# Kernel tuning notes

Measured on AMD Instinct MI355X. Metric: run time of the kernel, lower is better.

## Reference

```python
import jax, jax.numpy as jnp
import numpy as np

NH = 16
NKV = 4
ROPE_BASE = 10000.0
ROPE_TSL = 1024
EPS = 1.1920928955078125e-07  # torch fp32 finfo eps (F.rms_norm default)


def _rms_norm(t):
    return t * jax.lax.rsqrt(jnp.mean(t * t, axis=-1, keepdims=True) + EPS)


def _rope_tables(T, hd):
    # Rotary with rd = hd (rope_dims=0 -> full-head rope). NTK rescale if T > tsl.
    rd = hd
    if T > ROPE_TSL:
        base = ROPE_BASE * (T / ROPE_TSL) ** (rd / (rd - 2))
    else:
        base = ROPE_BASE
    inv_freq = 1.0 / base ** (np.arange(0, rd, 2, dtype=np.float32) / rd)
    t = np.arange(T, dtype=np.float32)
    fr = np.outer(t, inv_freq)  # [T, hd//2]
    return jnp.asarray(np.cos(fr)), jnp.asarray(np.sin(fr))


def _apply_rope(x, cos, sin):
    # x: [B,T,H,D]; cos/sin: [T, D//2] broadcast over batch & heads
    h = x.shape[-1] // 2
    x1, x2 = x[..., :h], x[..., h:]
    c = cos[None, :, None, :]
    s = sin[None, :, None, :]
    return jnp.concatenate((x1 * c + x2 * s, -x1 * s + x2 * c), axis=-1)


def setup_inputs() -> dict:
    key = jax.random.key(0)
    k1, k2, k3, k4, k5 = jax.random.split(key, 5)
    B, T, dim = 2, 2048, 2048
    hd = dim // NH
    kd = NKV * hd
    std = 0.02
    return {
        "x": jax.random.normal(k1, (B, T, dim), dtype=jnp.float32),
        "Wq": jax.random.normal(k2, (dim, dim), dtype=jnp.float32) * std,
        "Wk": jax.random.normal(k3, (kd, dim), dtype=jnp.float32) * std,
        "Wv": jax.random.normal(k4, (kd, dim), dtype=jnp.float32) * std,
        "Wp": jax.random.normal(k5, (dim, dim), dtype=jnp.float32) * std,
        "q_gain": jnp.full((NH,), 1.5, dtype=jnp.float32),
    }


def reference(x, Wq, Wk, Wv, Wp, q_gain):
    B, T, d = x.shape
    hd = d // NH
    g = NH // NKV
    q = (x @ Wq.T).reshape(B, T, NH, hd)
    k = (x @ Wk.T).reshape(B, T, NKV, hd)
    v = (x @ Wv.T).reshape(B, T, NKV, hd)
    q = _rms_norm(q)
    k = _rms_norm(k)
    cos, sin = _rope_tables(T, hd)
    q = _apply_rope(q, cos, sin)
    k = _apply_rope(k, cos, sin)
    q = q * q_gain[None, None, :, None]
    # GQA causal SDPA: group queries per kv head
    qg = q.reshape(B, T, NKV, g, hd)
    scores = jnp.einsum("btkgd,bskd->bkgts", qg, k) / jnp.sqrt(jnp.asarray(hd, x.dtype))
    causal = jnp.tril(jnp.ones((T, T), dtype=bool))
    scores = jnp.where(causal[None, None, None, :, :], scores, jnp.asarray(-jnp.inf, scores.dtype))
    attn = jax.nn.softmax(scores, axis=-1)
    y = jnp.einsum("bkgts,bskd->btkgd", attn, v).reshape(B, T, d)
    return y @ Wp.T
```

## Files before the change

### kernel.cpp

```cpp
#include <hip/hip_runtime.h>
#include <math.h>

#define NH 16
#define NKV 4
#define HD 128
#define DIM 2048
#define GQ 4
#define EPS 1.1920928955078125e-07f

typedef unsigned short u16;
using bf16x8 = __attribute__((ext_vector_type(8))) short;
using f16x4  = __attribute__((ext_vector_type(4))) _Float16;
using f32x4  = __attribute__((ext_vector_type(4))) float;

__device__ inline float fast_exp2(float x) { return __builtin_amdgcn_exp2f(x); }

__device__ inline short f2bf(float f) {
    unsigned u = __builtin_bit_cast(unsigned, f);
    return (short)((u + 0x7FFFu + ((u >> 16) & 1u)) >> 16);
}
__device__ inline u16 f2h(float f) {
    _Float16 h = (_Float16)f;
    return __builtin_bit_cast(u16, h);
}

#define ASYNC_LOAD16(g, l)                                                        \
    __builtin_amdgcn_global_load_lds(                                             \
        (const __attribute__((address_space(1))) unsigned*)(g),                   \
        (__attribute__((address_space(3))) unsigned*)(l), 16, 0, 0)

#define SCHED_FENCE() __builtin_amdgcn_sched_barrier(0)
#define WAIT_LGKM0()  asm volatile("s_waitcnt lgkmcnt(0)" ::: "memory")
#define WAIT_VM(N)    asm volatile("s_waitcnt vmcnt(" #N ")" ::: "memory")

__global__ __launch_bounds__(256) void cvt_bf16(const float* __restrict__ src,
                                                u16* __restrict__ dst, int n4) {
    int i = blockIdx.x * 256 + threadIdx.x;
    if (i < n4) {
        float4 f = ((const float4*)src)[i];
        ushort4 o;
        o.x = (u16)f2bf(f.x); o.y = (u16)f2bf(f.y);
        o.z = (u16)f2bf(f.z); o.w = (u16)f2bf(f.w);
        ((ushort4*)dst)[i] = o;
    }
}

__global__ __launch_bounds__(64) void rope_tab(float* __restrict__ ct,
                                               float* __restrict__ st,
                                               double base) {
    const int t = blockIdx.x;
    const int j = threadIdx.x;
    const float inv_freq = (float)pow(base, -(double)j / 64.0);
    const float fr = (float)t * inv_freq;
    ct[t * 64 + j] = cosf(fr);
    st[t * 64 + j] = sinf(fr);
}

#define BM 256
#define BN 256
#define BKT 64
#define NKT (DIM / BKT)

template <int EPI>
__global__ __launch_bounds__(512, 2) void gemm256(
    const u16* __restrict__ A, const u16* __restrict__ W,
    float* __restrict__ C, int N,
    u16* __restrict__ q16, u16* __restrict__ k16,
    u16* __restrict__ vt16,
    const float* __restrict__ ctab, const float* __restrict__ stab,
    const float* __restrict__ q_gain, int T) {
    __shared__ u16 As[2][BM * BKT];
    __shared__ u16 Bs[2][BN * BKT];

    const int tid  = threadIdx.x;
    const int wid  = tid >> 6;
    const int lane = tid & 63;
    const int l16  = lane & 15;
    const int quad = lane >> 4;
    const int wm   = wid >> 1;
    const int wn   = wid & 1;
    const int m0   = blockIdx.x * BM;
    const int n0   = blockIdx.y * BN;
    const int K    = DIM;

    const int srow = lane >> 3;
    const int scol = ((lane & 7) ^ srow) * 8;
    const u16* pa = A + (size_t)(m0 + srow) * K + scol;
    const u16* pw = W + (size_t)(n0 + srow) * K + scol;

    const int ca0 = ((quad)     ^ (l16 & 7)) * 8;
    const int ca1 = ((4 + quad) ^ (l16 & 7)) * 8;

    f32x4 acc[4][8];
#pragma unroll
    for (int i = 0; i < 4; i++)
#pragma unroll
        for (int j = 0; j < 8; j++) acc[i][j] = (f32x4){0.f, 0.f, 0.f, 0.f};

#pragma unroll
    for (int r = 0; r < 4; r++)
        ASYNC_LOAD16(pa + (size_t)(r * 64 + wid * 8) * K, &As[0][(r * 64 + wid * 8) * BKT]);
    ASYNC_LOAD16(pw + (size_t)(0 * 64 + wid * 8) * K, &Bs[0][(0 * 64 + wid * 8) * BKT]);
    ASYNC_LOAD16(pw + (size_t)(2 * 64 + wid * 8) * K, &Bs[0][(2 * 64 + wid * 8) * BKT]);
    ASYNC_LOAD16(pw + (size_t)(1 * 64 + wid * 8) * K, &Bs[0][(1 * 64 + wid * 8) * BKT]);
    ASYNC_LOAD16(pw + (size_t)(3 * 64 + wid * 8) * K, &Bs[0][(3 * 64 + wid * 8) * BKT]);
    WAIT_VM(2);
    SCHED_FENCE();
    __builtin_amdgcn_s_barrier();
    SCHED_FENCE();

#pragma unroll 1
    for (int kt = 0; kt < NKT; kt++) {
        const int cur = kt & 1;
        const u16* Ac = &As[cur][0];
        const u16* Bc = &Bs[cur][0];
        u16* An = &As[cur ^ 1][0];
        u16* Bn = &Bs[cur ^ 1][0];
        const size_t ko = (size_t)((kt + 1) & (NKT - 1)) * BKT;

        bf16x8 a0[4], a1[4];

        {
            bf16x8 bf[4];
#pragma unroll
            for (int mt = 0; mt < 4; mt++)
                a0[mt] = *(const bf16x8*)&Ac[(wm * 64 + mt * 16 + l16) * BKT + ca0];
#pragma unroll
            for (int nt = 0; nt < 4; nt++)
                bf[nt] = *(const bf16x8*)&Bc[(wn * 128 + nt * 16 + l16) * BKT + ca0];
#pragma unroll
            for (int r = 0; r < 4; r++)
                ASYNC_LOAD16(pa + (size_t)(r * 64 + wid * 8) * K + ko,
                             &An[(r * 64 + wid * 8) * BKT]);
            SCHED_FENCE();
            __builtin_amdgcn_s_barrier();
            WAIT_LGKM0();
            SCHED_FENCE();
            __builtin_amdgcn_s_setprio(1);
#pragma unroll
            for (int mt = 0; mt < 4; mt++)
#pragma unroll
                for (int nt = 0; nt < 4; nt++)
                    acc[mt][nt] = __builtin_amdgcn_mfma_f32_16x16x32_bf16(
                        a0[mt], bf[nt], acc[mt][nt], 0, 0, 0);
            __builtin_amdgcn_s_setprio(0);
            SCHED_FENCE();
            __builtin_amdgcn_s_barrier();
        }

        {
            bf16x8 bf[4];
#pragma unroll
            for (int mt = 0; mt < 4; mt++)
                a1[mt] = *(const bf16x8*)&Ac[(wm * 64 + mt * 16 + l16) * BKT + ca1];
#pragma unroll
            for (int nt = 0; nt < 4; nt++)
                bf[nt] = *(const bf16x8*)&Bc[(wn * 128 + nt * 16 + l16) * BKT + ca1];
            ASYNC_LOAD16(pw + (size_t)(0 * 64 + wid * 8) * K + ko,
                         &Bn[(0 * 64 + wid * 8) * BKT]);
            ASYNC_LOAD16(pw + (size_t)(2 * 64 + wid * 8) * K + ko,
                         &Bn[(2 * 64 + wid * 8) * BKT]);
            SCHED_FENCE();
            __builtin_amdgcn_s_barrier();
            WAIT_LGKM0();
            SCHED_FENCE();
            __builtin_amdgcn_s_setprio(1);
#pragma unroll
            for (int mt = 0; mt < 4; mt++)
#pragma unroll
                for (int nt = 0; nt < 4; nt++)
                    acc[mt][nt] = __builtin_amdgcn_mfma_f32_16x16x32_bf16(
                        a1[mt], bf[nt], acc[mt][nt], 0, 0, 0);
            __builtin_amdgcn_s_setprio(0);
            WAIT_VM(6);
            SCHED_FENCE();
            __builtin_amdgcn_s_barrier();
            SCHED_FENCE();
        }

        {
            bf16x8 bf[4];
#pragma unroll
            for (int nt = 0; nt < 4; nt++)
                bf[nt] = *(const bf16x8*)&Bc[(wn * 128 + (nt + 4) * 16 + l16) * BKT + ca0];
            ASYNC_LOAD16(pw + (size_t)(1 * 64 + wid * 8) * K + ko,
                         &Bn[(1 * 64 + wid * 8) * BKT]);
            ASYNC_LOAD16(pw + (size_t)(3 * 64 + wid * 8) * K + ko,
                         &Bn[(3 * 64 + wid * 8) * BKT]);
            SCHED_FENCE();
            __builtin_amdgcn_s_barrier();
            WAIT_LGKM0();
            SCHED_FENCE();
            __builtin_amdgcn_s_setprio(1);
#pragma unroll
            for (int mt = 0; mt < 4; mt++)
#pragma unroll
                for (int nt = 0; nt < 4; nt++)
                    acc[mt][nt + 4] = __builtin_amdgcn_mfma_f32_16x16x32_bf16(
                        a0[mt], bf[nt], acc[mt][nt + 4], 0, 0, 0);
            __builtin_amdgcn_s_setprio(0);
            SCHED_FENCE();
            __builtin_amdgcn_s_barrier();
        }

        {
            bf16x8 bf[4];
#pragma unroll
            for (int nt = 0; nt < 4; nt++)
                bf[nt] = *(const bf16x8*)&Bc[(wn * 128 + (nt + 4) * 16 + l16) * BKT + ca1];
            SCHED_FENCE();
            __builtin_amdgcn_s_barrier();
            WAIT_LGKM0();
            SCHED_FENCE();
            __builtin_amdgcn_s_setprio(1);
#pragma unroll
            for (int mt = 0; mt < 4; mt++)
#pragma unroll
                for (int nt = 0; nt < 4; nt++)
                    acc[mt][nt + 4] = __builtin_amdgcn_mfma_f32_16x16x32_bf16(
                        a1[mt], bf[nt], acc[mt][nt + 4], 0, 0, 0);
            __builtin_amdgcn_s_setprio(0);
            WAIT_VM(2);
            SCHED_FENCE();
            __builtin_amdgcn_s_barrier();
            SCHED_FENCE();
        }
    }
    WAIT_VM(0);

    if constexpr (EPI == 0) {
#pragma unroll
        for (int mt = 0; mt < 4; mt++)
#pragma unroll
            for (int nt = 0; nt < 8; nt++)
#pragma unroll
                for (int r = 0; r < 4; r++)
                    C[(size_t)(m0 + wm * 64 + mt * 16 + quad * 4 + r) * N +
                      n0 + wn * 128 + nt * 16 + l16] = acc[mt][nt][r];
    } else {
        const int nb = n0 + wn * 128;
        if (nb < 2560) {
            const bool isQ = (nb < 2048);
            const float gval =
                isQ ? (q_gain[nb >> 7] * 0.08838834764831843f * 1.4426950408889634f)
                    : 1.0f;
#pragma unroll
            for (int mt = 0; mt < 4; mt++) {
#pragma unroll
                for (int r = 0; r < 4; r++) {
                    float s = 0.f;
#pragma unroll
                    for (int nt = 0; nt < 8; nt++) {
                        float a = acc[mt][nt][r];
                        s = fmaf(a, a, s);
                    }
                    s += __shfl_xor(s, 1);
                    s += __shfl_xor(s, 2);
                    s += __shfl_xor(s, 4);
                    s += __shfl_xor(s, 8);
                    const float scale = rsqrtf(s * (1.0f / HD) + EPS) * gval;
                    const int m = m0 + wm * 64 + mt * 16 + quad * 4 + r;
                    const int t = m & (T - 1);
                    const float* ct = ctab + t * 64;
                    const float* st = stab + t * 64;
                    u16* dst = isQ ? (q16 + (size_t)m * 2048 + nb)
                                   : (k16 + (size_t)m * 512 + (nb - 2048));
#pragma unroll
                    for (int nt = 0; nt < 4; nt++) {
                        const int j = nt * 16 + l16;
                        const float c = ct[j], sn = st[j];
                        const float x1 = acc[mt][nt][r] * scale;
                        const float x2 = acc[mt][nt + 4][r] * scale;
                        dst[j]      = (u16)f2bf(x1 * c + x2 * sn);
                        dst[j + 64] = (u16)f2bf(x2 * c - x1 * sn);
                    }
                }
            }
        } else {
#pragma unroll
            for (int mt = 0; mt < 4; mt++) {
                const int mb = m0 + wm * 64 + mt * 16 + quad * 4;
                const int b = mb >> 11;
                const int t0 = mb & (T - 1);
#pragma unroll
                for (int nt = 0; nt < 8; nt++) {
                    const int dcol = nb - 2560 + nt * 16 + l16;
                    const int kvh = dcol >> 7;
                    const int d = dcol & (HD - 1);
                    ushort4 o;
                    o.x = f2h(acc[mt][nt][0]);
                    o.y = f2h(acc[mt][nt][1]);
                    o.z = f2h(acc[mt][nt][2]);
                    o.w = f2h(acc[mt][nt][3]);
                    *(ushort4*)(vt16 + ((size_t)((b * NKV + kvh) * HD + d)) * T + t0) = o;
                }
            }
        }
    }
}

#define QT 64
#define SK 64

__global__ __launch_bounds__(256) void flash4(const u16* __restrict__ q16,
                                              const u16* __restrict__ k16,
                                              const u16* __restrict__ vt16,
                                              u16* __restrict__ y16, int T) {
    __shared__ u16 Ks[2][SK * 128];
    __shared__ u16 Vt[2][HD * 64];

    const int tid = threadIdx.x;
    const int wave = tid >> 6;
    const int lane = tid & 63;
    const int l16 = lane & 15;
    const int quad = lane >> 4;

    const int bid = blockIdx.x;
    const int bh = bid & 31;
    const int pr = bid >> 5;
    const int h = bh & 15;
    const int b = bh >> 4;
    const int kv = h / GQ;

    const u16* kg = k16 + ((size_t)b * T * NKV + kv) * HD;
    const u16* vg = vt16 + (size_t)(b * NKV + kv) * HD * T;

    const int krow_in_seg = lane >> 4;
    const int kclog_base = lane & 15;
    const int vrow_in_seg = lane >> 3;
    const int vclog = (lane & 7) ^ (lane >> 3);

#pragma unroll 1
    for (int half = 0; half < 2; half++) {
        const int qt = half ? (T / QT - 1 - pr) : pr;
        const int q0 = qt * QT;
        const int qglob = q0 + wave * 16 + l16;
        const int nts = q0 / SK + 1;

        bf16x8 qf[4];
        {
            const u16* qp = q16 + ((size_t)(b * T + qglob) * NH + h) * HD;
#pragma unroll
            for (int kc = 0; kc < 4; kc++)
                qf[kc] = *(const bf16x8*)(qp + kc * 32 + quad * 8);
        }

        f32x4 of[8];
#pragma unroll
        for (int i = 0; i < 8; i++) of[i] = (f32x4){0.f, 0.f, 0.f, 0.f};
        float m_i = -1e30f, l_i = 0.0f;

        __syncthreads();
#pragma unroll
        for (int j = 0; j < 4; j++) {
            const int seg = wave * 4 + j;
            const int r = seg * 4 + krow_in_seg;
            const int clog = kclog_base ^ (r & 15);
            ASYNC_LOAD16(kg + (size_t)r * (NKV * HD) + clog * 8, &Ks[0][seg * 512]);
            const int d = seg * 8 + vrow_in_seg;
            ASYNC_LOAD16(vg + (size_t)d * T + vclog * 8, &Vt[0][seg * 512]);
        }

        for (int it = 0; it < nts; it++) {
            const int cur = it & 1;
            __syncthreads();

            if (it + 1 < nts) {
                const int s1 = (it + 1) * SK;
#pragma unroll
                for (int j = 0; j < 4; j++) {
                    const int seg = wave * 4 + j;
                    const int r = seg * 4 + krow_in_seg;
                    const int clog = kclog_base ^ (r & 15);
                    ASYNC_LOAD16(kg + (size_t)(s1 + r) * (NKV * HD) + clog * 8,
                                 &Ks[cur ^ 1][seg * 512]);
                    const int d = seg * 8 + vrow_in_seg;
                    ASYNC_LOAD16(vg + (size_t)d * T + s1 + vclog * 8,
                                 &Vt[cur ^ 1][seg * 512]);
                }
            }

            f32x4 sf[4];
#pragma unroll
            for (int st = 0; st < 4; st++) sf[st] = (f32x4){0.f, 0.f, 0.f, 0.f};
#pragma unroll
            for (int kc = 0; kc < 4; kc++)
#pragma unroll
                for (int st = 0; st < 4; st++) {
                    const int row = st * 16 + l16;
                    bf16x8 kf = *(const bf16x8*)
                        &Ks[cur][row * 128 + (((kc * 4 + quad) ^ l16) * 8)];
                    sf[st] = __builtin_amdgcn_mfma_f32_16x16x32_bf16(kf, qf[kc], sf[st], 0, 0, 0);
                }

            if (it == nts - 1) {
#pragma unroll
                for (int st = 0; st < 4; st++)
#pragma unroll
                    for (int r = 0; r < 4; r++)
                        if (q0 + st * 16 + quad * 4 + r > qglob) sf[st][r] = -1e30f;
            }

            float tm = -1e30f;
#pragma unroll
            for (int st = 0; st < 4; st++)
#pragma unroll
                for (int r = 0; r < 4; r++) tm = fmaxf(tm, sf[st][r]);
            tm = fmaxf(tm, __shfl_xor(tm, 16));
            tm = fmaxf(tm, __shfl_xor(tm, 32));

            const float mprev = m_i;
            const float mnew = fmaxf(mprev, tm);
            m_i = mnew;
            const float alpha = fast_exp2(mprev - mnew);

            f16x4 pf[4];
            float ls = 0.0f;
#pragma unroll
            for (int st = 0; st < 4; st++)
#pragma unroll
                for (int r = 0; r < 4; r++) {
                    float e = fast_exp2(sf[st][r] - mnew);
                    ls += e;
                    pf[st][r] = (_Float16)e;
                }
            ls += __shfl_xor(ls, 16);
            ls += __shfl_xor(ls, 32);
            l_i = alpha * l_i + ls;

            if (__ballot(mnew > mprev)) {
#pragma unroll
                for (int dt = 0; dt < 8; dt++)
#pragma unroll
                    for (int r = 0; r < 4; r++) of[dt][r] *= alpha;
            }

#pragma unroll
            for (int st = 0; st < 4; st++) {
                const int clog = st * 2 + (quad >> 1);
#pragma unroll
                for (int dt = 0; dt < 8; dt++) {
                    const int d = dt * 16 + l16;
                    const int phys = clog ^ (l16 & 7);
                    f16x4 va = *(const f16x4*)
                        &Vt[cur][d * 64 + phys * 8 + (quad & 1) * 4];
                    of[dt] = __builtin_amdgcn_mfma_f32_16x16x16f16(va, pf[st], of[dt], 0, 0, 0);
                }
            }
        }

        const float inv = 1.0f / l_i;
        u16* yp = y16 + ((size_t)(b * T + qglob) * NH + h) * HD + quad * 4;
#pragma unroll
        for (int dt = 0; dt < 8; dt++) {
            ushort4 o;
            o.x = (u16)f2bf(of[dt][0] * inv);
            o.y = (u16)f2bf(of[dt][1] * inv);
            o.z = (u16)f2bf(of[dt][2] * inv);
            o.w = (u16)f2bf(of[dt][3] * inv);
            *(ushort4*)(yp + dt * 16) = o;
        }
    }
}

extern "C" void kernel_launch(void* const* d_in, const int* in_sizes, int n_in,
                              void* d_out, int out_size, void* d_ws, size_t ws_size,
                              hipStream_t stream) {
    const float* x      = (const float*)d_in[0];
    const float* Wq     = (const float*)d_in[1];
    const float* Wk     = (const float*)d_in[2];
    const float* Wv     = (const float*)d_in[3];
    const float* Wp     = (const float*)d_in[4];
    const float* q_gain = (const float*)d_in[5];
    float* out = (float*)d_out;

    const int B = 2;
    const int BT = in_sizes[0] / DIM;
    const int T = BT / B;
    const int KD = NKV * HD;

    u16* x16   = (u16*)d_ws;
    u16* wqkv  = x16 + (size_t)BT * DIM;
    u16* wp16  = wqkv + (size_t)3072 * DIM;
    u16* q16   = wp16 + (size_t)DIM * DIM;
    u16* k16   = q16 + (size_t)BT * DIM;
    u16* vt16  = k16 + (size_t)BT * KD;
    float* ctab = (float*)(vt16 + (size_t)BT * KD);
    float* stab = ctab + (size_t)T * 64;
    u16* y16   = x16;

    double base = 10000.0;
    if (T > 1024) base = 10000.0 * pow((double)T / 1024.0, 128.0 / 126.0);

    const int nx4  = BT * DIM / 4;
    const int nwq4 = DIM * DIM / 4;
    const int nwk4 = KD * DIM / 4;

    cvt_bf16<<<(nx4 + 255) / 256, 256, 0, stream>>>(x, x16, nx4);
    cvt_bf16<<<(nwq4 + 255) / 256, 256, 0, stream>>>(Wq, wqkv, nwq4);
    cvt_bf16<<<(nwk4 + 255) / 256, 256, 0, stream>>>(Wk, wqkv + (size_t)2048 * DIM, nwk4);
    cvt_bf16<<<(nwk4 + 255) / 256, 256, 0, stream>>>(Wv, wqkv + (size_t)2560 * DIM, nwk4);
    cvt_bf16<<<(nwq4 + 255) / 256, 256, 0, stream>>>(Wp, wp16, nwq4);
    rope_tab<<<T, 64, 0, stream>>>(ctab, stab, base);

    gemm256<1><<<dim3(BT / BM, 3072 / BN), 512, 0, stream>>>(
        x16, wqkv, nullptr, 0, q16, k16, vt16, ctab, stab, q_gain, T);

    flash4<<<32 * (T / QT / 2), 256, 0, stream>>>(q16, k16, vt16, y16, T);

    gemm256<0><<<dim3(BT / BM, DIM / 128 / 2), 512, 0, stream>>>(
        y16, wp16, out, DIM, nullptr, nullptr, nullptr, nullptr, nullptr, nullptr, T);
}
```

Measured before the change: 324.8 us.

## Fuse conversion kernels, retile attention to 128-row blocks, shrink output GEMM tile

The five fp32-to-bf16 conversion launches become one fused kernel, and the rope table uses exp2 with a wider launch. The GEMM is templated on M-tile height, and the output projection now uses 128-row tiles so more blocks are in flight. Attention moves to 512-thread blocks of 128 queries, with each wave skipping the masked-out last KV tile, and a lazy rescale that only updates the running max when it grows by more than 8. Together these aim to cut launch overhead, raise occupancy and reduce softmax rescaling, at the risk of fp16 overflow headroom from the lazy max and a new load-balance pattern.

```diff
diff --git a/kernel.cpp b/kernel.cpp
--- a/kernel.cpp
+++ b/kernel.cpp
@@ -33,35 +33,65 @@
 #define WAIT_LGKM0()  asm volatile("s_waitcnt lgkmcnt(0)" ::: "memory")
 #define WAIT_VM(N)    asm volatile("s_waitcnt vmcnt(" #N ")" ::: "memory")
 
-__global__ __launch_bounds__(256) void cvt_bf16(const float* __restrict__ src,
-                                                u16* __restrict__ dst, int n4) {
+__global__ __launch_bounds__(256) void cvt_fused(
+    const float* __restrict__ x,  const float* __restrict__ wq,
+    const float* __restrict__ wk, const float* __restrict__ wv,
+    const float* __restrict__ wp,
+    u16* __restrict__ x16, u16* __restrict__ wqkv, u16* __restrict__ wp16,
+    int nx4, int total) {
     int i = blockIdx.x * 256 + threadIdx.x;
-    if (i < n4) {
-        float4 f = ((const float4*)src)[i];
-        ushort4 o;
-        o.x = (u16)f2bf(f.x); o.y = (u16)f2bf(f.y);
-        o.z = (u16)f2bf(f.z); o.w = (u16)f2bf(f.w);
-        ((ushort4*)dst)[i] = o;
-    }
-}
-
-__global__ __launch_bounds__(64) void rope_tab(float* __restrict__ ct,
-                                               float* __restrict__ st,
-                                               double base) {
-    const int t = blockIdx.x;
-    const int j = threadIdx.x;
-    const float inv_freq = (float)pow(base, -(double)j / 64.0);
+    if (i >= total) return;
+    const int nw4 = DIM * DIM / 4;
+    const int nk4 = (NKV * HD) * DIM / 4;
+    const float4* s4;
+    ushort4* d4;
+    if (i < nx4) {
+        s4 = (const float4*)x + i; d4 = (ushort4*)x16 + i;
+    } else {
+        int j = i - nx4;
+        if (j < nw4) {
+            s4 = (const float4*)wq + j; d4 = (ushort4*)wqkv + j;
+        } else {
+            j -= nw4;
+            if (j < nk4) {
+                s4 = (const float4*)wk + j;
+                d4 = (ushort4*)wqkv + (size_t)2048 * DIM / 4 + j;
+            } else {
+                j -= nk4;
+                if (j < nk4) {
+                    s4 = (const float4*)wv + j;
+                    d4 = (ushort4*)wqkv + (size_t)2560 * DIM / 4 + j;
+                } else {
+                    j -= nk4;
+                    s4 = (const float4*)wp + j; d4 = (ushort4*)wp16 + j;
+                }
+            }
+        }
+    }
+    float4 f = *s4;
+    ushort4 o;
+    o.x = (u16)f2bf(f.x); o.y = (u16)f2bf(f.y);
+    o.z = (u16)f2bf(f.z); o.w = (u16)f2bf(f.w);
+    *d4 = o;
+}
+
+__global__ __launch_bounds__(256) void rope_tab(float* __restrict__ ct,
+                                                float* __restrict__ st,
+                                                float l2b64) {
+    const int idx = blockIdx.x * 256 + threadIdx.x;
+    const int t = idx >> 6;
+    const int j = idx & 63;
+    const float inv_freq = fast_exp2(-(float)j * l2b64);
     const float fr = (float)t * inv_freq;
-    ct[t * 64 + j] = cosf(fr);
-    st[t * 64 + j] = sinf(fr);
-}
-
-#define BM 256
+    ct[idx] = cosf(fr);
+    st[idx] = sinf(fr);
+}
+
 #define BN 256
 #define BKT 64
 #define NKT (DIM / BKT)
 
-template <int EPI>
+template <int EPI, int MT>
 __global__ __launch_bounds__(512, 2) void gemm256(
     const u16* __restrict__ A, const u16* __restrict__ W,
     float* __restrict__ C, int N,
@@ -69,7 +99,7 @@
     u16* __restrict__ vt16,
     const float* __restrict__ ctab, const float* __restrict__ stab,
     const float* __restrict__ q_gain, int T) {
-    __shared__ u16 As[2][BM * BKT];
+    __shared__ u16 As[2][MT * 64 * BKT];
     __shared__ u16 Bs[2][BN * BKT];
 
     const int tid  = threadIdx.x;
@@ -79,7 +109,7 @@
     const int quad = lane >> 4;
     const int wm   = wid >> 1;
     const int wn   = wid & 1;
-    const int m0   = blockIdx.x * BM;
+    const int m0   = blockIdx.x * (MT * 64);
     const int n0   = blockIdx.y * BN;
     const int K    = DIM;
 
@@ -91,14 +121,14 @@
     const int ca0 = ((quad)     ^ (l16 & 7)) * 8;
     const int ca1 = ((4 + quad) ^ (l16 & 7)) * 8;
 
-    f32x4 acc[4][8];
-#pragma unroll
-    for (int i = 0; i < 4; i++)
+    f32x4 acc[MT][8];
+#pragma unroll
+    for (int i = 0; i < MT; i++)
 #pragma unroll
         for (int j = 0; j < 8; j++) acc[i][j] = (f32x4){0.f, 0.f, 0.f, 0.f};
 
 #pragma unroll
-    for (int r = 0; r < 4; r++)
+    for (int r = 0; r < MT; r++)
         ASYNC_LOAD16(pa + (size_t)(r * 64 + wid * 8) * K, &As[0][(r * 64 + wid * 8) * BKT]);
     ASYNC_LOAD16(pw + (size_t)(0 * 64 + wid * 8) * K, &Bs[0][(0 * 64 + wid * 8) * BKT]);
     ASYNC_LOAD16(pw + (size_t)(2 * 64 + wid * 8) * K, &Bs[0][(2 * 64 + wid * 8) * BKT]);
@@ -118,18 +148,18 @@
         u16* Bn = &Bs[cur ^ 1][0];
         const size_t ko = (size_t)((kt + 1) & (NKT - 1)) * BKT;
 
-        bf16x8 a0[4], a1[4];
+        bf16x8 a0[MT], a1[MT];
 
         {
             bf16x8 bf[4];
 #pragma unroll
-            for (int mt = 0; mt < 4; mt++)
-                a0[mt] = *(const bf16x8*)&Ac[(wm * 64 + mt * 16 + l16) * BKT + ca0];
+            for (int mt = 0; mt < MT; mt++)
+                a0[mt] = *(const bf16x8*)&Ac[(wm * (MT * 16) + mt * 16 + l16) * BKT + ca0];
 #pragma unroll
             for (int nt = 0; nt < 4; nt++)
                 bf[nt] = *(const bf16x8*)&Bc[(wn * 128 + nt * 16 + l16) * BKT + ca0];
 #pragma unroll
-            for (int r = 0; r < 4; r++)
+            for (int r = 0; r < MT; r++)
                 ASYNC_LOAD16(pa + (size_t)(r * 64 + wid * 8) * K + ko,
                              &An[(r * 64 + wid * 8) * BKT]);
             SCHED_FENCE();
@@ -138,7 +168,7 @@
             SCHED_FENCE();
             __builtin_amdgcn_s_setprio(1);
 #pragma unroll
-            for (int mt = 0; mt < 4; mt++)
+            for (int mt = 0; mt < MT; mt++)
 #pragma unroll
                 for (int nt = 0; nt < 4; nt++)
                     acc[mt][nt] = __builtin_amdgcn_mfma_f32_16x16x32_bf16(
@@ -151,8 +181,8 @@
         {
             bf16x8 bf[4];
 #pragma unroll
-            for (int mt = 0; mt < 4; mt++)
-                a1[mt] = *(const bf16x8*)&Ac[(wm * 64 + mt * 16 + l16) * BKT + ca1];
+            for (int mt = 0; mt < MT; mt++)
+                a1[mt] = *(const bf16x8*)&Ac[(wm * (MT * 16) + mt * 16 + l16) * BKT + ca1];
 #pragma unroll
             for (int nt = 0; nt < 4; nt++)
                 bf[nt] = *(const bf16x8*)&Bc[(wn * 128 + nt * 16 + l16) * BKT + ca1];
@@ -166,13 +196,13 @@
             SCHED_FENCE();
             __builtin_amdgcn_s_setprio(1);
 #pragma unroll
-            for (int mt = 0; mt < 4; mt++)
+            for (int mt = 0; mt < MT; mt++)
 #pragma unroll
                 for (int nt = 0; nt < 4; nt++)
                     acc[mt][nt] = __builtin_amdgcn_mfma_f32_16x16x32_bf16(
                         a1[mt], bf[nt], acc[mt][nt], 0, 0, 0);
             __builtin_amdgcn_s_setprio(0);
-            WAIT_VM(6);
+            if constexpr (MT == 4) { WAIT_VM(6); } else { WAIT_VM(4); }
             SCHED_FENCE();
             __builtin_amdgcn_s_barrier();
             SCHED_FENCE();
@@ -193,7 +223,7 @@
             SCHED_FENCE();
             __builtin_amdgcn_s_setprio(1);
 #pragma unroll
-            for (int mt = 0; mt < 4; mt++)
+            for (int mt = 0; mt < MT; mt++)
 #pragma unroll
                 for (int nt = 0; nt < 4; nt++)
                     acc[mt][nt + 4] = __builtin_amdgcn_mfma_f32_16x16x32_bf16(
@@ -214,7 +244,7 @@
             SCHED_FENCE();
             __builtin_amdgcn_s_setprio(1);
 #pragma unroll
-            for (int mt = 0; mt < 4; mt++)
+            for (int mt = 0; mt < MT; mt++)
 #pragma unroll
                 for (int nt = 0; nt < 4; nt++)
                     acc[mt][nt + 4] = __builtin_amdgcn_mfma_f32_16x16x32_bf16(
@@ -230,12 +260,12 @@
 
     if constexpr (EPI == 0) {
 #pragma unroll
-        for (int mt = 0; mt < 4; mt++)
+        for (int mt = 0; mt < MT; mt++)
 #pragma unroll
             for (int nt = 0; nt < 8; nt++)
 #pragma unroll
                 for (int r = 0; r < 4; r++)
-                    C[(size_t)(m0 + wm * 64 + mt * 16 + quad * 4 + r) * N +
+                    C[(size_t)(m0 + wm * (MT * 16) + mt * 16 + quad * 4 + r) * N +
                       n0 + wn * 128 + nt * 16 + l16] = acc[mt][nt][r];
     } else {
         const int nb = n0 + wn * 128;
@@ -245,7 +275,7 @@
                 isQ ? (q_gain[nb >> 7] * 0.08838834764831843f * 1.4426950408889634f)
                     : 1.0f;
 #pragma unroll
-            for (int mt = 0; mt < 4; mt++) {
+            for (int mt = 0; mt < MT; mt++) {
 #pragma unroll
                 for (int r = 0; r < 4; r++) {
                     float s = 0.f;
@@ -259,7 +289,7 @@
                     s += __shfl_xor(s, 4);
                     s += __shfl_xor(s, 8);
                     const float scale = rsqrtf(s * (1.0f / HD) + EPS) * gval;
-                    const int m = m0 + wm * 64 + mt * 16 + quad * 4 + r;
+                    const int m = m0 + wm * (MT * 16) + mt * 16 + quad * 4 + r;
                     const int t = m & (T - 1);
                     const float* ct = ctab + t * 64;
                     const float* st = stab + t * 64;
@@ -278,8 +308,8 @@
             }
         } else {
 #pragma unroll
-            for (int mt = 0; mt < 4; mt++) {
-                const int mb = m0 + wm * 64 + mt * 16 + quad * 4;
+            for (int mt = 0; mt < MT; mt++) {
+                const int mb = m0 + wm * (MT * 16) + mt * 16 + quad * 4;
                 const int b = mb >> 11;
                 const int t0 = mb & (T - 1);
 #pragma unroll
@@ -299,10 +329,10 @@
     }
 }
 
-#define QT 64
+#define QT 128
 #define SK 64
 
-__global__ __launch_bounds__(256) void flash4(const u16* __restrict__ q16,
+__global__ __launch_bounds__(512) void flash5(const u16* __restrict__ q16,
                                               const u16* __restrict__ k16,
                                               const u16* __restrict__ vt16,
                                               u16* __restrict__ y16, int T) {
@@ -317,7 +347,9 @@
 
     const int bid = blockIdx.x;
     const int bh = bid & 31;
-    const int pr = bid >> 5;
+    const int qi = bid >> 5;
+    const int nqt = T / QT;
+    const int qt = (qi < (nqt >> 1)) ? qi : (nqt - 1 - (qi - (nqt >> 1)));
     const int h = bh & 15;
     const int b = bh >> 4;
     const int kv = h / GQ;
@@ -330,136 +362,133 @@
     const int vrow_in_seg = lane >> 3;
     const int vclog = (lane & 7) ^ (lane >> 3);
 
-#pragma unroll 1
-    for (int half = 0; half < 2; half++) {
-        const int qt = half ? (T / QT - 1 - pr) : pr;
-        const int q0 = qt * QT;
-        const int qglob = q0 + wave * 16 + l16;
-        const int nts = q0 / SK + 1;
-
-        bf16x8 qf[4];
-        {
-            const u16* qp = q16 + ((size_t)(b * T + qglob) * NH + h) * HD;
-#pragma unroll
-            for (int kc = 0; kc < 4; kc++)
-                qf[kc] = *(const bf16x8*)(qp + kc * 32 + quad * 8);
-        }
-
-        f32x4 of[8];
-#pragma unroll
-        for (int i = 0; i < 8; i++) of[i] = (f32x4){0.f, 0.f, 0.f, 0.f};
-        float m_i = -1e30f, l_i = 0.0f;
-
+    const int q0 = qt * QT;
+    const int qglob = q0 + wave * 16 + l16;
+    const int nts = q0 / SK + 2;
+
+    bf16x8 qf[4];
+    {
+        const u16* qp = q16 + ((size_t)(b * T + qglob) * NH + h) * HD;
+#pragma unroll
+        for (int kc = 0; kc < 4; kc++)
+            qf[kc] = *(const bf16x8*)(qp + kc * 32 + quad * 8);
+    }
+
+    f32x4 of[8];
+#pragma unroll
+    for (int i = 0; i < 8; i++) of[i] = (f32x4){0.f, 0.f, 0.f, 0.f};
+    float m_i = -1e30f, l_i = 0.0f;
+
+#pragma unroll
+    for (int j = 0; j < 2; j++) {
+        const int seg = wave * 2 + j;
+        const int r = seg * 4 + krow_in_seg;
+        const int clog = kclog_base ^ (r & 15);
+        ASYNC_LOAD16(kg + (size_t)r * (NKV * HD) + clog * 8, &Ks[0][seg * 512]);
+        const int d = seg * 8 + vrow_in_seg;
+        ASYNC_LOAD16(vg + (size_t)d * T + vclog * 8, &Vt[0][seg * 512]);
+    }
+
+    for (int it = 0; it < nts; it++) {
+        const int cur = it & 1;
         __syncthreads();
-#pragma unroll
-        for (int j = 0; j < 4; j++) {
-            const int seg = wave * 4 + j;
-            const int r = seg * 4 + krow_in_seg;
-            const int clog = kclog_base ^ (r & 15);
-            ASYNC_LOAD16(kg + (size_t)r * (NKV * HD) + clog * 8, &Ks[0][seg * 512]);
-            const int d = seg * 8 + vrow_in_seg;
-            ASYNC_LOAD16(vg + (size_t)d * T + vclog * 8, &Vt[0][seg * 512]);
-        }
-
-        for (int it = 0; it < nts; it++) {
-            const int cur = it & 1;
-            __syncthreads();
-
-            if (it + 1 < nts) {
-                const int s1 = (it + 1) * SK;
-#pragma unroll
-                for (int j = 0; j < 4; j++) {
-                    const int seg = wave * 4 + j;
-                    const int r = seg * 4 + krow_in_seg;
-                    const int clog = kclog_base ^ (r & 15);
-                    ASYNC_LOAD16(kg + (size_t)(s1 + r) * (NKV * HD) + clog * 8,
-                                 &Ks[cur ^ 1][seg * 512]);
-                    const int d = seg * 8 + vrow_in_seg;
-                    ASYNC_LOAD16(vg + (size_t)d * T + s1 + vclog * 8,
-                                 &Vt[cur ^ 1][seg * 512]);
-                }
-            }
-
-            f32x4 sf[4];
-#pragma unroll
-            for (int st = 0; st < 4; st++) sf[st] = (f32x4){0.f, 0.f, 0.f, 0.f};
-#pragma unroll
-            for (int kc = 0; kc < 4; kc++)
-#pragma unroll
-                for (int st = 0; st < 4; st++) {
-                    const int row = st * 16 + l16;
-                    bf16x8 kf = *(const bf16x8*)
-                        &Ks[cur][row * 128 + (((kc * 4 + quad) ^ l16) * 8)];
-                    sf[st] = __builtin_amdgcn_mfma_f32_16x16x32_bf16(kf, qf[kc], sf[st], 0, 0, 0);
-                }
-
-            if (it == nts - 1) {
-#pragma unroll
-                for (int st = 0; st < 4; st++)
-#pragma unroll
-                    for (int r = 0; r < 4; r++)
-                        if (q0 + st * 16 + quad * 4 + r > qglob) sf[st][r] = -1e30f;
-            }
-
-            float tm = -1e30f;
+
+        if (it + 1 < nts) {
+            const int s1 = (it + 1) * SK;
+#pragma unroll
+            for (int j = 0; j < 2; j++) {
+                const int seg = wave * 2 + j;
+                const int r = seg * 4 + krow_in_seg;
+                const int clog = kclog_base ^ (r & 15);
+                ASYNC_LOAD16(kg + (size_t)(s1 + r) * (NKV * HD) + clog * 8,
+                             &Ks[cur ^ 1][seg * 512]);
+                const int d = seg * 8 + vrow_in_seg;
+                ASYNC_LOAD16(vg + (size_t)d * T + s1 + vclog * 8,
+                             &Vt[cur ^ 1][seg * 512]);
+            }
+        }
+
+        if (it == nts - 1 && wave < 4) continue;
+
+        f32x4 sf[4];
+#pragma unroll
+        for (int st = 0; st < 4; st++) sf[st] = (f32x4){0.f, 0.f, 0.f, 0.f};
+#pragma unroll
+        for (int kc = 0; kc < 4; kc++)
+#pragma unroll
+            for (int st = 0; st < 4; st++) {
+                const int row = st * 16 + l16;
+                bf16x8 kf = *(const bf16x8*)
+                    &Ks[cur][row * 128 + (((kc * 4 + quad) ^ l16) * 8)];
+                sf[st] = __builtin_amdgcn_mfma_f32_16x16x32_bf16(kf, qf[kc], sf[st], 0, 0, 0);
+            }
+
+        if (it >= nts - 2) {
+            const int s0 = it * SK;
 #pragma unroll
             for (int st = 0; st < 4; st++)
 #pragma unroll
-                for (int r = 0; r < 4; r++) tm = fmaxf(tm, sf[st][r]);
-            tm = fmaxf(tm, __shfl_xor(tm, 16));
-            tm = fmaxf(tm, __shfl_xor(tm, 32));
-
-            const float mprev = m_i;
-            const float mnew = fmaxf(mprev, tm);
+                for (int r = 0; r < 4; r++)
+                    if (s0 + st * 16 + quad * 4 + r > qglob) sf[st][r] = -1e30f;
+        }
+
+        float tm = -1e30f;
+#pragma unroll
+        for (int st = 0; st < 4; st++)
+#pragma unroll
+            for (int r = 0; r < 4; r++) tm = fmaxf(tm, sf[st][r]);
+        tm = fmaxf(tm, __shfl_xor(tm, 16));
+        tm = fmaxf(tm, __shfl_xor(tm, 32));
+
+        if (__ballot(tm > m_i + 8.0f)) {
+            const float mnew = fmaxf(m_i, tm);
+            const float alpha = fast_exp2(m_i - mnew);
             m_i = mnew;
-            const float alpha = fast_exp2(mprev - mnew);
-
-            f16x4 pf[4];
-            float ls = 0.0f;
-#pragma unroll
-            for (int st = 0; st < 4; st++)
-#pragma unroll
-                for (int r = 0; r < 4; r++) {
-                    float e = fast_exp2(sf[st][r] - mnew);
-                    ls += e;
-                    pf[st][r] = (_Float16)e;
-                }
-            ls += __shfl_xor(ls, 16);
-            ls += __shfl_xor(ls, 32);
-            l_i = alpha * l_i + ls;
-
-            if (__ballot(mnew > mprev)) {
-#pragma unroll
-                for (int dt = 0; dt < 8; dt++)
-#pragma unroll
-                    for (int r = 0; r < 4; r++) of[dt][r] *= alpha;
-            }
-
-#pragma unroll
-            for (int st = 0; st < 4; st++) {
-                const int clog = st * 2 + (quad >> 1);
-#pragma unroll
-                for (int dt = 0; dt < 8; dt++) {
-                    const int d = dt * 16 + l16;
-                    const int phys = clog ^ (l16 & 7);
-                    f16x4 va = *(const f16x4*)
-                        &Vt[cur][d * 64 + phys * 8 + (quad & 1) * 4];
-                    of[dt] = __builtin_amdgcn_mfma_f32_16x16x16f16(va, pf[st], of[dt], 0, 0, 0);
-                }
-            }
-        }
-
-        const float inv = 1.0f / l_i;
-        u16* yp = y16 + ((size_t)(b * T + qglob) * NH + h) * HD + quad * 4;
-#pragma unroll
-        for (int dt = 0; dt < 8; dt++) {
-            ushort4 o;
-            o.x = (u16)f2bf(of[dt][0] * inv);
-            o.y = (u16)f2bf(of[dt][1] * inv);
-            o.z = (u16)f2bf(of[dt][2] * inv);
-            o.w = (u16)f2bf(of[dt][3] * inv);
-            *(ushort4*)(yp + dt * 16) = o;
-        }
+            l_i *= alpha;
+#pragma unroll
+            for (int dt = 0; dt < 8; dt++)
+#pragma unroll
+                for (int r = 0; r < 4; r++) of[dt][r] *= alpha;
+        }
+
+        f16x4 pf[4];
+        float ls = 0.0f;
+#pragma unroll
+        for (int st = 0; st < 4; st++)
+#pragma unroll
+            for (int r = 0; r < 4; r++) {
+                float e = fast_exp2(sf[st][r] - m_i);
+                ls += e;
+                pf[st][r] = (_Float16)e;
+            }
+        ls += __shfl_xor(ls, 16);
+        ls += __shfl_xor(ls, 32);
+        l_i += ls;
+
+#pragma unroll
+        for (int st = 0; st < 4; st++) {
+            const int clog = st * 2 + (quad >> 1);
+#pragma unroll
+            for (int dt = 0; dt < 8; dt++) {
+                const int d = dt * 16 + l16;
+                const int phys = clog ^ (l16 & 7);
+                f16x4 va = *(const f16x4*)
+                    &Vt[cur][d * 64 + phys * 8 + (quad & 1) * 4];
+                of[dt] = __builtin_amdgcn_mfma_f32_16x16x16f16(va, pf[st], of[dt], 0, 0, 0);
+            }
+        }
+    }
+
+    const float inv = 1.0f / l_i;
+    u16* yp = y16 + ((size_t)(b * T + qglob) * NH + h) * HD + quad * 4;
+#pragma unroll
+    for (int dt = 0; dt < 8; dt++) {
+        ushort4 o;
+        o.x = (u16)f2bf(of[dt][0] * inv);
+        o.y = (u16)f2bf(of[dt][1] * inv);
+        o.z = (u16)f2bf(of[dt][2] * inv);
+        o.w = (u16)f2bf(of[dt][3] * inv);
+        *(ushort4*)(yp + dt * 16) = o;
     }
 }
 
@@ -491,23 +520,20 @@
 
     double base = 10000.0;
     if (T > 1024) base = 10000.0 * pow((double)T / 1024.0, 128.0 / 126.0);
+    const float l2b64 = (float)(log2(base) / 64.0);
 
     const int nx4  = BT * DIM / 4;
-    const int nwq4 = DIM * DIM / 4;
-    const int nwk4 = KD * DIM / 4;
-
-    cvt_bf16<<<(nx4 + 255) / 256, 256, 0, stream>>>(x, x16, nx4);
-    cvt_bf16<<<(nwq4 + 255) / 256, 256, 0, stream>>>(Wq, wqkv, nwq4);
-    cvt_bf16<<<(nwk4 + 255) / 256, 256, 0, stream>>>(Wk, wqkv + (size_t)2048 * DIM, nwk4);
-    cvt_bf16<<<(nwk4 + 255) / 256, 256, 0, stream>>>(Wv, wqkv + (size_t)2560 * DIM, nwk4);
-    cvt_bf16<<<(nwq4 + 255) / 256, 256, 0, stream>>>(Wp, wp16, nwq4);
-    rope_tab<<<T, 64, 0, stream>>>(ctab, stab, base);
-
-    gemm256<1><<<dim3(BT / BM, 3072 / BN), 512, 0, stream>>>(
+    const int total4 = nx4 + 2 * (DIM * DIM / 4) + 2 * (KD * DIM / 4);
+
+    cvt_fused<<<(total4 + 255) / 256, 256, 0, stream>>>(
+        x, Wq, Wk, Wv, Wp, x16, wqkv, wp16, nx4, total4);
+    rope_tab<<<(T * 64 + 255) / 256, 256, 0, stream>>>(ctab, stab, l2b64);
+
+    gemm256<1, 4><<<dim3(BT / 256, 3072 / BN), 512, 0, stream>>>(
         x16, wqkv, nullptr, 0, q16, k16, vt16, ctab, stab, q_gain, T);
 
-    flash4<<<32 * (T / QT / 2), 256, 0, stream>>>(q16, k16, vt16, y16, T);
-
-    gemm256<0><<<dim3(BT / BM, DIM / 128 / 2), 512, 0, stream>>>(
+    flash5<<<32 * (T / QT), 512, 0, stream>>>(q16, k16, vt16, y16, T);
+
+    gemm256<0, 2><<<dim3(BT / 128, DIM / BN), 512, 0, stream>>>(
         y16, wp16, out, DIM, nullptr, nullptr, nullptr, nullptr, nullptr, nullptr, T);
 }
```

Result: faster. 304.0 us (-6.4%).
